# Kernel tuning notes

Hardware: AMD Instinct MI355X
Metric: run time of the kernel (lower is better)

Reference implementation:

```python
import jax, jax.numpy as jnp
import numpy as np

B, N, IN_DIM, OUT_DIM, C = 8, 8192, 1024, 512, 64
TEMPERATURE = 1.0
LN_EPS = 1e-5


def setup_inputs() -> dict:
    key = jax.random.key(0)
    ks = jax.random.split(key, 6)
    node_embeddings = jax.random.normal(ks[0], (B, N, IN_DIM), dtype=jnp.float32)
    node_mask = jnp.zeros((B, N), dtype=bool)  # True => node is masked out
    # xavier_uniform for cluster_centers [C, OUT_DIM]
    lim_c = float(np.sqrt(6.0 / (C + OUT_DIM)))
    cluster_centers = jax.random.uniform(ks[1], (C, OUT_DIM), jnp.float32, -lim_c, lim_c)
    # nn.Linear default init (kaiming-uniform-ish bounds)
    lim_n = float(1.0 / np.sqrt(IN_DIM))
    W_node = jax.random.uniform(ks[2], (IN_DIM, OUT_DIM), jnp.float32, -lim_n, lim_n)
    b_node = jax.random.uniform(ks[3], (OUT_DIM,), jnp.float32, -lim_n, lim_n)
    lim_k = float(1.0 / np.sqrt(OUT_DIM))
    W_cluster = jax.random.uniform(ks[4], (OUT_DIM, OUT_DIM), jnp.float32, -lim_k, lim_k)
    b_cluster = jax.random.uniform(ks[5], (OUT_DIM,), jnp.float32, -lim_k, lim_k)
    ln_gamma = jnp.ones((OUT_DIM,), jnp.float32)
    ln_beta = jnp.zeros((OUT_DIM,), jnp.float32)
    return {
        "node_embeddings": node_embeddings,
        "node_mask": node_mask,
        "cluster_centers": cluster_centers,
        "W_node": W_node,
        "b_node": b_node,
        "W_cluster": W_cluster,
        "b_cluster": b_cluster,
        "ln_gamma": ln_gamma,
        "ln_beta": ln_beta,
    }


def reference(node_embeddings, node_mask, cluster_centers, W_node, b_node,
              W_cluster, b_cluster, ln_gamma, ln_beta):
    # node projection: [B, N, D]
    node_proj = jnp.einsum('bni,io->bno', node_embeddings, W_node) + b_node
    # projected cluster centers (batch-independent): [C, D]
    ccp = cluster_centers @ W_cluster + b_cluster
    # similarities: [B, C, N]
    sims = jnp.einsum('cd,bnd->bcn', ccp, node_proj) / TEMPERATURE
    sims = jnp.where(node_mask[:, None, :], -jnp.inf, sims)
    assignment_weights = jax.nn.softmax(sims, axis=-1)  # dropout is identity in eval
    # aggregate: [B, C, D], residual add of projected centers
    compressed = jnp.einsum('bcn,bnd->bcd', assignment_weights, node_proj) + ccp
    # LayerNorm over last dim
    mu = jnp.mean(compressed, axis=-1, keepdims=True)
    var = jnp.var(compressed, axis=-1, keepdims=True)
    compressed = (compressed - mu) * jax.lax.rsqrt(var + LN_EPS) * ln_gamma + ln_beta
    return compressed, assignment_weights
```

## Files before the change

### kernel.cpp

```cpp
#include <hip/hip_runtime.h>
#include <hip/hip_bf16.h>
#include <math.h>

#define Bn 8
#define Nn 8192
#define KIN 1024
#define DOUT 512
#define NC 64
#define LN_EPS 1e-5f

typedef short bf16x8 __attribute__((ext_vector_type(8)));
typedef short s8v __attribute__((ext_vector_type(8)));
typedef short s4v __attribute__((ext_vector_type(4)));
typedef float f32x4 __attribute__((ext_vector_type(4)));

__device__ __forceinline__ short f2bf(float f) {
    __hip_bfloat16 h = __float2bfloat16(f);
    return __builtin_bit_cast(short, h);
}

__device__ __forceinline__ void load_lds16(const void* g, void* l) {
    __builtin_amdgcn_global_load_lds(
        (const __attribute__((address_space(1))) unsigned int*)g,
        (__attribute__((address_space(3))) unsigned int*)l, 16, 0, 0);
}

__global__ __launch_bounds__(256) void k_prep_w(const float* __restrict__ W,
                                                short* __restrict__ Wt) {
    __shared__ short L[64 * 72];
    const int tid = threadIdx.x;
    const int kt = blockIdx.x >> 3, nt = blockIdx.x & 7;
    const int k0 = kt * 64, n0 = nt * 64;
    {
        int r = tid >> 2, c0 = (tid & 3) * 16;
        const float* g = W + (size_t)(k0 + r) * DOUT + n0 + c0;
        float4 a0 = *reinterpret_cast<const float4*>(g);
        float4 a1 = *reinterpret_cast<const float4*>(g + 4);
        float4 a2 = *reinterpret_cast<const float4*>(g + 8);
        float4 a3 = *reinterpret_cast<const float4*>(g + 12);
        s8v p0, p1;
        p0[0]=f2bf(a0.x); p0[1]=f2bf(a0.y); p0[2]=f2bf(a0.z); p0[3]=f2bf(a0.w);
        p0[4]=f2bf(a1.x); p0[5]=f2bf(a1.y); p0[6]=f2bf(a1.z); p0[7]=f2bf(a1.w);
        p1[0]=f2bf(a2.x); p1[1]=f2bf(a2.y); p1[2]=f2bf(a2.z); p1[3]=f2bf(a2.w);
        p1[4]=f2bf(a3.x); p1[5]=f2bf(a3.y); p1[6]=f2bf(a3.z); p1[7]=f2bf(a3.w);
        *reinterpret_cast<s8v*>(&L[r * 72 + c0]) = p0;
        *reinterpret_cast<s8v*>(&L[r * 72 + c0 + 8]) = p1;
    }
    __syncthreads();
    {
        int n = tid >> 2, kc = (tid & 3) * 16;
        s8v y0, y1;
#pragma unroll
        for (int j = 0; j < 8; ++j) y0[j] = L[(kc + j) * 72 + n];
#pragma unroll
        for (int j = 0; j < 8; ++j) y1[j] = L[(kc + 8 + j) * 72 + n];
        short* o = Wt + (size_t)(n0 + n) * KIN + k0 + kc;
        *reinterpret_cast<s8v*>(o) = y0;
        *reinterpret_cast<s8v*>(o + 8) = y1;
    }
}

__global__ __launch_bounds__(256) void k_prep_c(
    const float* __restrict__ cc, const float* __restrict__ Wc,
    const float* __restrict__ bc, float* __restrict__ ccp_f,
    short* __restrict__ ccp_bf) {
    __shared__ float ccs[512];
    const int tid = threadIdx.x, c = blockIdx.x;
    ccs[tid] = cc[c * DOUT + tid];
    ccs[tid + 256] = cc[c * DOUT + tid + 256];
    __syncthreads();
    float a0 = bc[tid], a1 = bc[tid + 256];
    for (int k = 0; k < DOUT; ++k) {
        float s = ccs[k];
        a0 += s * Wc[(size_t)k * DOUT + tid];
        a1 += s * Wc[(size_t)k * DOUT + tid + 256];
    }
    ccp_f[c * DOUT + tid] = a0;
    ccp_f[c * DOUT + tid + 256] = a1;
    ccp_bf[c * DOUT + tid] = f2bf(a0);
    ccp_bf[c * DOUT + tid + 256] = f2bf(a1);
}

__global__ __launch_bounds__(256, 2) void k_gemm1(
    const float* __restrict__ A, const short* __restrict__ Wt,
    const float* __restrict__ bias, short* __restrict__ proj,
    short* __restrict__ projT) {
    __shared__ short As[64 * 40];
    __shared__ short Bs[512 * 32];
    const int tid = threadIdx.x, lane = tid & 63, wv = tid >> 6;
    const int quad = lane >> 4, l15 = lane & 15;
    const int m0 = blockIdx.x * 64;

    f32x4 acc[4][8];
#pragma unroll
    for (int i = 0; i < 4; ++i)
#pragma unroll
        for (int j = 0; j < 8; ++j) acc[i][j] = (f32x4){0.f, 0.f, 0.f, 0.f};

    const int ar = tid >> 2;
    const int ac = (tid & 2) * 8;
    const int ac2 = (tid & 3) * 8;
    const float* Ag = A + (size_t)(m0 + ar) * KIN + ac2;

    for (int it = 0; it < KIN / 32; ++it) {
        const int k0 = it * 32;
        __syncthreads();
        {
            float4 a0 = *reinterpret_cast<const float4*>(Ag + k0);
            float4 a1 = *reinterpret_cast<const float4*>(Ag + k0 + 4);
            s8v p;
            p[0]=f2bf(a0.x); p[1]=f2bf(a0.y); p[2]=f2bf(a0.z); p[3]=f2bf(a0.w);
            p[4]=f2bf(a1.x); p[5]=f2bf(a1.y); p[6]=f2bf(a1.z); p[7]=f2bf(a1.w);
            *reinterpret_cast<s8v*>(&As[ar * 40 + ac2]) = p;
        }
#pragma unroll
        for (int i = 0; i < 8; ++i) {
            int c = i * 256 + tid;
            int n = c >> 2, kc = c & 3;
            load_lds16(Wt + (size_t)n * KIN + k0 + kc * 8,
                       Bs + (i * 256 + wv * 64) * 8);
        }
        __syncthreads();
        bf16x8 af[4], bfr[8];
#pragma unroll
        for (int mi = 0; mi < 4; ++mi)
            af[mi] = *reinterpret_cast<const bf16x8*>(&As[(mi * 16 + l15) * 40 + quad * 8]);
#pragma unroll
        for (int ni = 0; ni < 8; ++ni)
            bfr[ni] = *reinterpret_cast<const bf16x8*>(&Bs[(wv * 128 + ni * 16 + l15) * 32 + quad * 8]);
#pragma unroll
        for (int mi = 0; mi < 4; ++mi)
#pragma unroll
            for (int ni = 0; ni < 8; ++ni)
                acc[mi][ni] = __builtin_amdgcn_mfma_f32_16x16x32_bf16(af[mi], bfr[ni], acc[mi][ni], 0, 0, 0);
    }
#pragma unroll
    for (int ni = 0; ni < 8; ++ni) {
        int col = wv * 128 + ni * 16 + l15;
        float bv = bias[col];
#pragma unroll
        for (int mi = 0; mi < 4; ++mi) {
            int row0 = m0 + mi * 16 + quad * 4;
            s4v t;
#pragma unroll
            for (int r = 0; r < 4; ++r) {
                short v = f2bf(acc[mi][ni][r] + bv);
                t[r] = v;
                proj[(size_t)(row0 + r) * DOUT + col] = v;
            }
            *reinterpret_cast<s4v*>(projT + (size_t)col * (Bn * Nn) + row0) = t;
        }
    }
}

__global__ __launch_bounds__(256) void k_sims(
    const short* __restrict__ ccp_bf, const short* __restrict__ proj,
    float* __restrict__ sims) {
    __shared__ short As[64 * 32];
    __shared__ short Bs[128 * 32];
    const int tid = threadIdx.x, lane = tid & 63, wv = tid >> 6;
    const int quad = lane >> 4, l15 = lane & 15;
    const int b = blockIdx.x >> 6, nt = blockIdx.x & 63;
    const int n0 = nt * 128;
    const int wm = wv & 1, wn = wv >> 1;

    f32x4 acc[2][4];
#pragma unroll
    for (int i = 0; i < 2; ++i)
#pragma unroll
        for (int j = 0; j < 4; ++j) acc[i][j] = (f32x4){0.f, 0.f, 0.f, 0.f};

    for (int it = 0; it < DOUT / 32; ++it) {
        const int k0 = it * 32;
        __syncthreads();
        {
#pragma unroll
            for (int i = 0; i < 2; ++i) {
                int c = i * 256 + tid;
                int r = c >> 2, kc = c & 3;
                load_lds16(ccp_bf + (size_t)r * DOUT + k0 + kc * 8,
                           As + (i * 256 + wv * 64) * 8);
            }
        }
#pragma unroll
        for (int i = 0; i < 2; ++i) {
            int c = i * 256 + tid;
            int r = c >> 2, kc = c & 3;
            load_lds16(proj + (size_t)(b * Nn + n0 + r) * DOUT + k0 + kc * 8,
                       Bs + (i * 256 + wv * 64) * 8);
        }
        __syncthreads();
        bf16x8 af[2], bfr[4];
#pragma unroll
        for (int mi = 0; mi < 2; ++mi)
            af[mi] = *reinterpret_cast<const bf16x8*>(&As[(wm * 32 + mi * 16 + l15) * 32 + quad * 8]);
#pragma unroll
        for (int ni = 0; ni < 4; ++ni)
            bfr[ni] = *reinterpret_cast<const bf16x8*>(&Bs[(wn * 64 + ni * 16 + l15) * 32 + quad * 8]);
#pragma unroll
        for (int mi = 0; mi < 2; ++mi)
#pragma unroll
            for (int ni = 0; ni < 4; ++ni)
                acc[mi][ni] = __builtin_amdgcn_mfma_f32_16x16x32_bf16(af[mi], bfr[ni], acc[mi][ni], 0, 0, 0);
    }
#pragma unroll
    for (int mi = 0; mi < 2; ++mi)
#pragma unroll
        for (int ni = 0; ni < 4; ++ni)
#pragma unroll
            for (int r = 0; r < 4; ++r) {
                int c = wm * 32 + mi * 16 + quad * 4 + r;
                int n = n0 + wn * 64 + ni * 16 + l15;
                sims[((size_t)b * NC + c) * Nn + n] = acc[mi][ni][r];
            }
}

__global__ __launch_bounds__(256) void k_softmax(
    float* __restrict__ aw, const unsigned char* __restrict__ mask,
    short* __restrict__ aw_bf) {
    __shared__ float red[8];
    const int tid = threadIdx.x, lane = tid & 63, wv = tid >> 6;
    const int b = blockIdx.x >> 6, c = blockIdx.x & 63;
    float* p = aw + ((size_t)b * NC + c) * Nn;
    short* q = aw_bf + ((size_t)b * NC + c) * Nn;
    const unsigned char* mp = mask + b * Nn;

    float v[32];
    float mx = -INFINITY;
#pragma unroll
    for (int i = 0; i < 32; ++i) {
        int idx = tid + i * 256;
        float x = p[idx];
        if (mp[idx]) x = -INFINITY;
        v[i] = x;
        mx = fmaxf(mx, x);
    }
    for (int off = 32; off; off >>= 1) mx = fmaxf(mx, __shfl_xor(mx, off));
    if (lane == 0) red[wv] = mx;
    __syncthreads();
    mx = fmaxf(fmaxf(red[0], red[1]), fmaxf(red[2], red[3]));
    __syncthreads();

    float s = 0.f;
#pragma unroll
    for (int i = 0; i < 32; ++i) {
        v[i] = expf(v[i] - mx);
        s += v[i];
    }
    for (int off = 32; off; off >>= 1) s += __shfl_xor(s, off);
    if (lane == 0) red[wv] = s;
    __syncthreads();
    s = red[0] + red[1] + red[2] + red[3];
    float inv = 1.f / s;
#pragma unroll
    for (int i = 0; i < 32; ++i) {
        int idx = tid + i * 256;
        float w = v[i] * inv;
        p[idx] = w;
        q[idx] = f2bf(w);
    }
}

__global__ __launch_bounds__(256) void k_agg(
    const short* __restrict__ aw_bf, const short* __restrict__ projT,
    float* __restrict__ partial) {
    __shared__ short As[64 * 32];
    __shared__ short Bs[128 * 32];
    const int tid = threadIdx.x, lane = tid & 63, wv = tid >> 6;
    const int quad = lane >> 4, l15 = lane & 15;
    const int b = blockIdx.x >> 5, dt = (blockIdx.x >> 3) & 3, ks = blockIdx.x & 7;
    const int d0 = dt * 128;
    const int wm = wv & 1, wn = wv >> 1;

    f32x4 acc[2][4];
#pragma unroll
    for (int i = 0; i < 2; ++i)
#pragma unroll
        for (int j = 0; j < 4; ++j) acc[i][j] = (f32x4){0.f, 0.f, 0.f, 0.f};

    for (int it = 0; it < 32; ++it) {
        const int nb = ks * 1024 + it * 32;
        __syncthreads();
#pragma unroll
        for (int i = 0; i < 2; ++i) {
            int c = i * 256 + tid;
            int r = c >> 2, kc = c & 3;
            load_lds16(aw_bf + ((size_t)b * NC + r) * Nn + nb + kc * 8,
                       As + (i * 256 + wv * 64) * 8);
        }
#pragma unroll
        for (int i = 0; i < 2; ++i) {
            int c = i * 256 + tid;
            int r = c >> 2, kc = c & 3;
            load_lds16(projT + (size_t)(d0 + r) * (Bn * Nn) + b * Nn + nb + kc * 8,
                       Bs + (i * 256 + wv * 64) * 8);
        }
        __syncthreads();
        bf16x8 af[2], bfr[4];
#pragma unroll
        for (int mi = 0; mi < 2; ++mi)
            af[mi] = *reinterpret_cast<const bf16x8*>(&As[(wm * 32 + mi * 16 + l15) * 32 + quad * 8]);
#pragma unroll
        for (int ni = 0; ni < 4; ++ni)
            bfr[ni] = *reinterpret_cast<const bf16x8*>(&Bs[(wn * 64 + ni * 16 + l15) * 32 + quad * 8]);
#pragma unroll
        for (int mi = 0; mi < 2; ++mi)
#pragma unroll
            for (int ni = 0; ni < 4; ++ni)
                acc[mi][ni] = __builtin_amdgcn_mfma_f32_16x16x32_bf16(af[mi], bfr[ni], acc[mi][ni], 0, 0, 0);
    }
#pragma unroll
    for (int mi = 0; mi < 2; ++mi)
#pragma unroll
        for (int ni = 0; ni < 4; ++ni)
#pragma unroll
            for (int r = 0; r < 4; ++r) {
                int c = wm * 32 + mi * 16 + quad * 4 + r;
                int d = d0 + wn * 64 + ni * 16 + l15;
                partial[(((size_t)b * 8 + ks) * NC + c) * DOUT + d] = acc[mi][ni][r];
            }
}

__global__ __launch_bounds__(256) void k_ln(
    const float* __restrict__ partial, const float* __restrict__ ccp,
    const float* __restrict__ gamma, const float* __restrict__ beta,
    float* __restrict__ out) {
    __shared__ float red[16];
    const int tid = threadIdx.x, lane = tid & 63, wv = tid >> 6;
    const int b = blockIdx.x >> 6, c = blockIdx.x & 63;
    float v0 = ccp[c * DOUT + tid], v1 = ccp[c * DOUT + tid + 256];
#pragma unroll
    for (int ks = 0; ks < 8; ++ks) {
        const float* pp = partial + (((size_t)b * 8 + ks) * NC + c) * DOUT;
        v0 += pp[tid];
        v1 += pp[tid + 256];
    }
    float s = v0 + v1, sq = v0 * v0 + v1 * v1;
    for (int off = 32; off; off >>= 1) {
        s += __shfl_xor(s, off);
        sq += __shfl_xor(sq, off);
    }
    if (lane == 0) { red[wv] = s; red[8 + wv] = sq; }
    __syncthreads();
    s = red[0] + red[1] + red[2] + red[3];
    sq = red[8] + red[9] + red[10] + red[11];
    float mu = s * (1.f / 512.f);
    float var = sq * (1.f / 512.f) - mu * mu;
    float rs = rsqrtf(var + LN_EPS);
    size_t base = ((size_t)b * NC + c) * DOUT;
    out[base + tid] = (v0 - mu) * rs * gamma[tid] + beta[tid];
    out[base + tid + 256] = (v1 - mu) * rs * gamma[tid + 256] + beta[tid + 256];
}

extern "C" void kernel_launch(void* const* d_in, const int* in_sizes, int n_in,
                              void* d_out, int out_size, void* d_ws, size_t ws_size,
                              hipStream_t stream) {
    const float* node_emb = (const float*)d_in[0];
    const unsigned char* mask = (const unsigned char*)d_in[1];
    const float* cc = (const float*)d_in[2];
    const float* Wn = (const float*)d_in[3];
    const float* bn = (const float*)d_in[4];
    const float* Wc = (const float*)d_in[5];
    const float* bc = (const float*)d_in[6];
    const float* gamma = (const float*)d_in[7];
    const float* beta = (const float*)d_in[8];
    float* out = (float*)d_out;

    char* ws = (char*)d_ws;
    short* proj   = (short*)(ws);
    short* projT  = (short*)(ws + 67108864);
    short* aw_bf  = (short*)(ws + 134217728);
    float* ccp_f  = (float*)(ws + 142606336);
    short* ccp_bf = (short*)(ws + 142737408);
    short* Wt     = (short*)(ws + 142802944);
    float* partial= (float*)(ws + 143851520);

    float* sims = out + (size_t)Bn * NC * DOUT;

    k_prep_w<<<128, 256, 0, stream>>>(Wn, Wt);
    k_prep_c<<<64, 256, 0, stream>>>(cc, Wc, bc, ccp_f, ccp_bf);
    k_gemm1<<<1024, 256, 0, stream>>>(node_emb, Wt, bn, proj, projT);
    k_sims<<<512, 256, 0, stream>>>(ccp_bf, proj, sims);
    k_softmax<<<512, 256, 0, stream>>>(sims, mask, aw_bf);
    k_agg<<<256, 256, 0, stream>>>(aw_bf, projT, partial);
    k_ln<<<512, 256, 0, stream>>>(partial, ccp_f, gamma, beta, out);
}
```

Measured before the change: 567.8 us.

## Drop LDS staging in GEMM kernels, vectorize softmax, split agg and prep wider

The three MFMA kernels (gemm1, sims, agg) stop staging tiles through shared memory and instead load MFMA fragments straight from global memory into registers, which removes the barriers and LDS traffic. The softmax kernel switches to float4 and uchar4 vectorized accesses. The agg kernel's N split goes from 8 to 16 chunks to double the grid, with layer-norm summing 16 partials, and k_prep_c splits each cluster's work across two blocks with four independent accumulators. The risk is that direct global fragment loads are strided and poorly coalesced, and each wave reloads data that the LDS tiles used to share, which raises L2 and HBM traffic in gemm1, whose time likely dominates.

```diff
diff --git a/kernel.cpp b/kernel.cpp
--- a/kernel.cpp
+++ b/kernel.cpp
@@ -19,10 +19,11 @@
     return __builtin_bit_cast(short, h);
 }
 
-__device__ __forceinline__ void load_lds16(const void* g, void* l) {
-    __builtin_amdgcn_global_load_lds(
-        (const __attribute__((address_space(1))) unsigned int*)g,
-        (__attribute__((address_space(3))) unsigned int*)l, 16, 0, 0);
+__device__ __forceinline__ bf16x8 cvt8(float4 u, float4 v) {
+    bf16x8 r;
+    r[0] = f2bf(u.x); r[1] = f2bf(u.y); r[2] = f2bf(u.z); r[3] = f2bf(u.w);
+    r[4] = f2bf(v.x); r[5] = f2bf(v.y); r[6] = f2bf(v.z); r[7] = f2bf(v.w);
+    return r;
 }
 
 __global__ __launch_bounds__(256) void k_prep_w(const float* __restrict__ W,
@@ -38,13 +39,8 @@
         float4 a1 = *reinterpret_cast<const float4*>(g + 4);
         float4 a2 = *reinterpret_cast<const float4*>(g + 8);
         float4 a3 = *reinterpret_cast<const float4*>(g + 12);
-        s8v p0, p1;
-        p0[0]=f2bf(a0.x); p0[1]=f2bf(a0.y); p0[2]=f2bf(a0.z); p0[3]=f2bf(a0.w);
-        p0[4]=f2bf(a1.x); p0[5]=f2bf(a1.y); p0[6]=f2bf(a1.z); p0[7]=f2bf(a1.w);
-        p1[0]=f2bf(a2.x); p1[1]=f2bf(a2.y); p1[2]=f2bf(a2.z); p1[3]=f2bf(a2.w);
-        p1[4]=f2bf(a3.x); p1[5]=f2bf(a3.y); p1[6]=f2bf(a3.z); p1[7]=f2bf(a3.w);
-        *reinterpret_cast<s8v*>(&L[r * 72 + c0]) = p0;
-        *reinterpret_cast<s8v*>(&L[r * 72 + c0 + 8]) = p1;
+        *reinterpret_cast<s8v*>(&L[r * 72 + c0]) = cvt8(a0, a1);
+        *reinterpret_cast<s8v*>(&L[r * 72 + c0 + 8]) = cvt8(a2, a3);
     }
     __syncthreads();
     {
@@ -65,28 +61,31 @@
     const float* __restrict__ bc, float* __restrict__ ccp_f,
     short* __restrict__ ccp_bf) {
     __shared__ float ccs[512];
-    const int tid = threadIdx.x, c = blockIdx.x;
+    const int tid = threadIdx.x;
+    const int c = blockIdx.x >> 1, d = (blockIdx.x & 1) * 256 + tid;
     ccs[tid] = cc[c * DOUT + tid];
     ccs[tid + 256] = cc[c * DOUT + tid + 256];
     __syncthreads();
-    float a0 = bc[tid], a1 = bc[tid + 256];
-    for (int k = 0; k < DOUT; ++k) {
-        float s = ccs[k];
-        a0 += s * Wc[(size_t)k * DOUT + tid];
-        a1 += s * Wc[(size_t)k * DOUT + tid + 256];
-    }
-    ccp_f[c * DOUT + tid] = a0;
-    ccp_f[c * DOUT + tid + 256] = a1;
-    ccp_bf[c * DOUT + tid] = f2bf(a0);
-    ccp_bf[c * DOUT + tid + 256] = f2bf(a1);
+    float a0 = bc[d], a1 = 0.f, a2 = 0.f, a3 = 0.f;
+    for (int k = 0; k < DOUT; k += 8) {
+        a0 += ccs[k + 0] * Wc[(size_t)(k + 0) * DOUT + d];
+        a1 += ccs[k + 1] * Wc[(size_t)(k + 1) * DOUT + d];
+        a2 += ccs[k + 2] * Wc[(size_t)(k + 2) * DOUT + d];
+        a3 += ccs[k + 3] * Wc[(size_t)(k + 3) * DOUT + d];
+        a0 += ccs[k + 4] * Wc[(size_t)(k + 4) * DOUT + d];
+        a1 += ccs[k + 5] * Wc[(size_t)(k + 5) * DOUT + d];
+        a2 += ccs[k + 6] * Wc[(size_t)(k + 6) * DOUT + d];
+        a3 += ccs[k + 7] * Wc[(size_t)(k + 7) * DOUT + d];
+    }
+    float a = (a0 + a1) + (a2 + a3);
+    ccp_f[c * DOUT + d] = a;
+    ccp_bf[c * DOUT + d] = f2bf(a);
 }
 
 __global__ __launch_bounds__(256, 2) void k_gemm1(
     const float* __restrict__ A, const short* __restrict__ Wt,
     const float* __restrict__ bias, short* __restrict__ proj,
     short* __restrict__ projT) {
-    __shared__ short As[64 * 40];
-    __shared__ short Bs[512 * 32];
     const int tid = threadIdx.x, lane = tid & 63, wv = tid >> 6;
     const int quad = lane >> 4, l15 = lane & 15;
     const int m0 = blockIdx.x * 64;
@@ -97,37 +96,21 @@
 #pragma unroll
         for (int j = 0; j < 8; ++j) acc[i][j] = (f32x4){0.f, 0.f, 0.f, 0.f};
 
-    const int ar = tid >> 2;
-    const int ac = (tid & 2) * 8;
-    const int ac2 = (tid & 3) * 8;
-    const float* Ag = A + (size_t)(m0 + ar) * KIN + ac2;
-
-    for (int it = 0; it < KIN / 32; ++it) {
-        const int k0 = it * 32;
-        __syncthreads();
-        {
-            float4 a0 = *reinterpret_cast<const float4*>(Ag + k0);
-            float4 a1 = *reinterpret_cast<const float4*>(Ag + k0 + 4);
-            s8v p;
-            p[0]=f2bf(a0.x); p[1]=f2bf(a0.y); p[2]=f2bf(a0.z); p[3]=f2bf(a0.w);
-            p[4]=f2bf(a1.x); p[5]=f2bf(a1.y); p[6]=f2bf(a1.z); p[7]=f2bf(a1.w);
-            *reinterpret_cast<s8v*>(&As[ar * 40 + ac2]) = p;
+    const float* Ab = A + (size_t)(m0 + l15) * KIN + quad * 8;
+    const short* Bb = Wt + (size_t)(wv * 128 + l15) * KIN + quad * 8;
+
+    for (int k0 = 0; k0 < KIN; k0 += 32) {
+        bf16x8 af[4], bfr[8];
+#pragma unroll
+        for (int mi = 0; mi < 4; ++mi) {
+            const float* p = Ab + (size_t)mi * 16 * KIN + k0;
+            float4 u = *reinterpret_cast<const float4*>(p);
+            float4 v = *reinterpret_cast<const float4*>(p + 4);
+            af[mi] = cvt8(u, v);
         }
 #pragma unroll
-        for (int i = 0; i < 8; ++i) {
-            int c = i * 256 + tid;
-            int n = c >> 2, kc = c & 3;
-            load_lds16(Wt + (size_t)n * KIN + k0 + kc * 8,
-                       Bs + (i * 256 + wv * 64) * 8);
-        }
-        __syncthreads();
-        bf16x8 af[4], bfr[8];
-#pragma unroll
-        for (int mi = 0; mi < 4; ++mi)
-            af[mi] = *reinterpret_cast<const bf16x8*>(&As[(mi * 16 + l15) * 40 + quad * 8]);
-#pragma unroll
         for (int ni = 0; ni < 8; ++ni)
-            bfr[ni] = *reinterpret_cast<const bf16x8*>(&Bs[(wv * 128 + ni * 16 + l15) * 32 + quad * 8]);
+            bfr[ni] = *reinterpret_cast<const bf16x8*>(Bb + (size_t)ni * 16 * KIN + k0);
 #pragma unroll
         for (int mi = 0; mi < 4; ++mi)
 #pragma unroll
@@ -156,8 +139,6 @@
 __global__ __launch_bounds__(256) void k_sims(
     const short* __restrict__ ccp_bf, const short* __restrict__ proj,
     float* __restrict__ sims) {
-    __shared__ short As[64 * 32];
-    __shared__ short Bs[128 * 32];
     const int tid = threadIdx.x, lane = tid & 63, wv = tid >> 6;
     const int quad = lane >> 4, l15 = lane & 15;
     const int b = blockIdx.x >> 6, nt = blockIdx.x & 63;
@@ -170,33 +151,17 @@
 #pragma unroll
         for (int j = 0; j < 4; ++j) acc[i][j] = (f32x4){0.f, 0.f, 0.f, 0.f};
 
-    for (int it = 0; it < DOUT / 32; ++it) {
-        const int k0 = it * 32;
-        __syncthreads();
-        {
-#pragma unroll
-            for (int i = 0; i < 2; ++i) {
-                int c = i * 256 + tid;
-                int r = c >> 2, kc = c & 3;
-                load_lds16(ccp_bf + (size_t)r * DOUT + k0 + kc * 8,
-                           As + (i * 256 + wv * 64) * 8);
-            }
-        }
-#pragma unroll
-        for (int i = 0; i < 2; ++i) {
-            int c = i * 256 + tid;
-            int r = c >> 2, kc = c & 3;
-            load_lds16(proj + (size_t)(b * Nn + n0 + r) * DOUT + k0 + kc * 8,
-                       Bs + (i * 256 + wv * 64) * 8);
-        }
-        __syncthreads();
+    const short* Ab = ccp_bf + (size_t)(wm * 32 + l15) * DOUT + quad * 8;
+    const short* Bb = proj + (size_t)(b * Nn + n0 + wn * 64 + l15) * DOUT + quad * 8;
+
+    for (int k0 = 0; k0 < DOUT; k0 += 32) {
         bf16x8 af[2], bfr[4];
 #pragma unroll
         for (int mi = 0; mi < 2; ++mi)
-            af[mi] = *reinterpret_cast<const bf16x8*>(&As[(wm * 32 + mi * 16 + l15) * 32 + quad * 8]);
+            af[mi] = *reinterpret_cast<const bf16x8*>(Ab + (size_t)mi * 16 * DOUT + k0);
 #pragma unroll
         for (int ni = 0; ni < 4; ++ni)
-            bfr[ni] = *reinterpret_cast<const bf16x8*>(&Bs[(wn * 64 + ni * 16 + l15) * 32 + quad * 8]);
+            bfr[ni] = *reinterpret_cast<const bf16x8*>(Bb + (size_t)ni * 16 * DOUT + k0);
 #pragma unroll
         for (int mi = 0; mi < 2; ++mi)
 #pragma unroll
@@ -221,19 +186,23 @@
     __shared__ float red[8];
     const int tid = threadIdx.x, lane = tid & 63, wv = tid >> 6;
     const int b = blockIdx.x >> 6, c = blockIdx.x & 63;
-    float* p = aw + ((size_t)b * NC + c) * Nn;
-    short* q = aw_bf + ((size_t)b * NC + c) * Nn;
-    const unsigned char* mp = mask + b * Nn;
-
-    float v[32];
+    float4* p4 = reinterpret_cast<float4*>(aw + ((size_t)b * NC + c) * Nn);
+    s4v* q4 = reinterpret_cast<s4v*>(aw_bf + ((size_t)b * NC + c) * Nn);
+    const uchar4* mp4 = reinterpret_cast<const uchar4*>(mask + (size_t)b * Nn);
+
+    float4 v[8];
     float mx = -INFINITY;
 #pragma unroll
-    for (int i = 0; i < 32; ++i) {
+    for (int i = 0; i < 8; ++i) {
         int idx = tid + i * 256;
-        float x = p[idx];
-        if (mp[idx]) x = -INFINITY;
+        float4 x = p4[idx];
+        uchar4 m = mp4[idx];
+        if (m.x) x.x = -INFINITY;
+        if (m.y) x.y = -INFINITY;
+        if (m.z) x.z = -INFINITY;
+        if (m.w) x.w = -INFINITY;
         v[i] = x;
-        mx = fmaxf(mx, x);
+        mx = fmaxf(mx, fmaxf(fmaxf(x.x, x.y), fmaxf(x.z, x.w)));
     }
     for (int off = 32; off; off >>= 1) mx = fmaxf(mx, __shfl_xor(mx, off));
     if (lane == 0) red[wv] = mx;
@@ -243,9 +212,11 @@
 
     float s = 0.f;
 #pragma unroll
-    for (int i = 0; i < 32; ++i) {
-        v[i] = expf(v[i] - mx);
-        s += v[i];
+    for (int i = 0; i < 8; ++i) {
+        v[i].x = expf(v[i].x - mx); s += v[i].x;
+        v[i].y = expf(v[i].y - mx); s += v[i].y;
+        v[i].z = expf(v[i].z - mx); s += v[i].z;
+        v[i].w = expf(v[i].w - mx); s += v[i].w;
     }
     for (int off = 32; off; off >>= 1) s += __shfl_xor(s, off);
     if (lane == 0) red[wv] = s;
@@ -253,22 +224,23 @@
     s = red[0] + red[1] + red[2] + red[3];
     float inv = 1.f / s;
 #pragma unroll
-    for (int i = 0; i < 32; ++i) {
+    for (int i = 0; i < 8; ++i) {
         int idx = tid + i * 256;
-        float w = v[i] * inv;
-        p[idx] = w;
-        q[idx] = f2bf(w);
+        float4 x = v[i];
+        x.x *= inv; x.y *= inv; x.z *= inv; x.w *= inv;
+        p4[idx] = x;
+        s4v t;
+        t[0] = f2bf(x.x); t[1] = f2bf(x.y); t[2] = f2bf(x.z); t[3] = f2bf(x.w);
+        q4[idx] = t;
     }
 }
 
 __global__ __launch_bounds__(256) void k_agg(
     const short* __restrict__ aw_bf, const short* __restrict__ projT,
     float* __restrict__ partial) {
-    __shared__ short As[64 * 32];
-    __shared__ short Bs[128 * 32];
     const int tid = threadIdx.x, lane = tid & 63, wv = tid >> 6;
     const int quad = lane >> 4, l15 = lane & 15;
-    const int b = blockIdx.x >> 5, dt = (blockIdx.x >> 3) & 3, ks = blockIdx.x & 7;
+    const int b = blockIdx.x >> 6, dt = (blockIdx.x >> 4) & 3, ks = blockIdx.x & 15;
     const int d0 = dt * 128;
     const int wm = wv & 1, wn = wv >> 1;
 
@@ -278,31 +250,18 @@
 #pragma unroll
         for (int j = 0; j < 4; ++j) acc[i][j] = (f32x4){0.f, 0.f, 0.f, 0.f};
 
-    for (int it = 0; it < 32; ++it) {
-        const int nb = ks * 1024 + it * 32;
-        __syncthreads();
-#pragma unroll
-        for (int i = 0; i < 2; ++i) {
-            int c = i * 256 + tid;
-            int r = c >> 2, kc = c & 3;
-            load_lds16(aw_bf + ((size_t)b * NC + r) * Nn + nb + kc * 8,
-                       As + (i * 256 + wv * 64) * 8);
-        }
-#pragma unroll
-        for (int i = 0; i < 2; ++i) {
-            int c = i * 256 + tid;
-            int r = c >> 2, kc = c & 3;
-            load_lds16(projT + (size_t)(d0 + r) * (Bn * Nn) + b * Nn + nb + kc * 8,
-                       Bs + (i * 256 + wv * 64) * 8);
-        }
-        __syncthreads();
+    const int nb0 = ks * 512;
+    const short* Ab = aw_bf + ((size_t)b * NC + wm * 32 + l15) * Nn + nb0 + quad * 8;
+    const short* Bb = projT + (size_t)(d0 + wn * 64 + l15) * (Bn * Nn) + b * Nn + nb0 + quad * 8;
+
+    for (int nb = 0; nb < 512; nb += 32) {
         bf16x8 af[2], bfr[4];
 #pragma unroll
         for (int mi = 0; mi < 2; ++mi)
-            af[mi] = *reinterpret_cast<const bf16x8*>(&As[(wm * 32 + mi * 16 + l15) * 32 + quad * 8]);
+            af[mi] = *reinterpret_cast<const bf16x8*>(Ab + (size_t)mi * 16 * Nn + nb);
 #pragma unroll
         for (int ni = 0; ni < 4; ++ni)
-            bfr[ni] = *reinterpret_cast<const bf16x8*>(&Bs[(wn * 64 + ni * 16 + l15) * 32 + quad * 8]);
+            bfr[ni] = *reinterpret_cast<const bf16x8*>(Bb + (size_t)ni * 16 * (Bn * Nn) + nb);
 #pragma unroll
         for (int mi = 0; mi < 2; ++mi)
 #pragma unroll
@@ -317,7 +276,7 @@
             for (int r = 0; r < 4; ++r) {
                 int c = wm * 32 + mi * 16 + quad * 4 + r;
                 int d = d0 + wn * 64 + ni * 16 + l15;
-                partial[(((size_t)b * 8 + ks) * NC + c) * DOUT + d] = acc[mi][ni][r];
+                partial[(((size_t)b * 16 + ks) * NC + c) * DOUT + d] = acc[mi][ni][r];
             }
 }
 
@@ -330,8 +289,8 @@
     const int b = blockIdx.x >> 6, c = blockIdx.x & 63;
     float v0 = ccp[c * DOUT + tid], v1 = ccp[c * DOUT + tid + 256];
 #pragma unroll
-    for (int ks = 0; ks < 8; ++ks) {
-        const float* pp = partial + (((size_t)b * 8 + ks) * NC + c) * DOUT;
+    for (int ks = 0; ks < 16; ++ks) {
+        const float* pp = partial + (((size_t)b * 16 + ks) * NC + c) * DOUT;
         v0 += pp[tid];
         v1 += pp[tid + 256];
     }
@@ -378,10 +337,10 @@
     float* sims = out + (size_t)Bn * NC * DOUT;
 
     k_prep_w<<<128, 256, 0, stream>>>(Wn, Wt);
-    k_prep_c<<<64, 256, 0, stream>>>(cc, Wc, bc, ccp_f, ccp_bf);
+    k_prep_c<<<128, 256, 0, stream>>>(cc, Wc, bc, ccp_f, ccp_bf);
     k_gemm1<<<1024, 256, 0, stream>>>(node_emb, Wt, bn, proj, projT);
     k_sims<<<512, 256, 0, stream>>>(ccp_bf, proj, sims);
     k_softmax<<<512, 256, 0, stream>>>(sims, mask, aw_bf);
-    k_agg<<<256, 256, 0, stream>>>(aw_bf, projT, partial);
+    k_agg<<<512, 256, 0, stream>>>(aw_bf, projT, partial);
     k_ln<<<512, 256, 0, stream>>>(partial, ccp_f, gamma, beta, out);
 }
```

After: 666.9 us. +17.5%, slower.
